# Optimization experiments

Measured on AMD Instinct MI355X. Metric: run time of the kernel, lower is better.

## Reference

```python
import jax, jax.numpy as jnp
import numpy as np

N = 50000      # num_nodes
DEG = 32       # fixed out-degree
E = N * DEG    # num graph edges
B = 1024       # num query edges (batch_size)
EPS = 1e-8
F_DROP = 0.7   # f_dropout used in random_fill


def _mlp(x, w1, b1, w2, b2):
    # Linear(1,d) -> ReLU -> Linear(d,1); x: [M,1]
    h = jax.nn.relu(x * w1[None, :] + b1[None, :])   # [M,d]
    return (h @ w2)[:, None] + b2                    # [M,1]


def setup_inputs() -> dict:
    key = jax.random.key(0)
    ks = jax.random.split(key, 20)
    inp = {
        'neighbors': jax.random.randint(ks[0], (N, DEG), 0, N, dtype=jnp.int32),
        'edge_w': jax.random.uniform(ks[1], (E,), dtype=jnp.float32),
        'src': jax.random.randint(ks[2], (B,), 0, N, dtype=jnp.int32),
        'dst': jax.random.randint(ks[3], (B,), 0, N, dtype=jnp.int32),
    }
    d = 64
    names = ['fe', 'fn', 'gp']
    i = 4
    for nm in names:
        s = 1.0 / np.sqrt(d)
        inp[nm + '_w1'] = jax.random.uniform(ks[i], (d,), minval=-1.0, maxval=1.0); i += 1
        inp[nm + '_b1'] = jax.random.uniform(ks[i], (d,), minval=-1.0, maxval=1.0); i += 1
        inp[nm + '_w2'] = jax.random.uniform(ks[i], (d,), minval=-s, maxval=s); i += 1
        inp[nm + '_b2'] = jax.random.uniform(ks[i], (1,), minval=-s, maxval=s); i += 1
    return inp


def reference(neighbors, edge_w, src, dst,
              fe_w1, fe_b1, fe_w2, fe_b2,
              fn_w1, fn_b1, fn_w2, fn_b2,
              gp_w1, gp_b1, gp_w2, gp_b2):
    # ---- node structural features: scatter_add of f_edge over edge dst ----
    cols = neighbors.reshape(-1)                                  # [E] edge dst (srcdst order)
    ew_A = _mlp(edge_w[:, None], fe_w1, fe_b1, fe_w2, fe_b2)      # [E,1]
    nsf = jnp.zeros((N, 1), dtype=ew_A.dtype).at[cols].add(ew_A)  # scatter_add -> [N,1]
    nsf = _mlp(nsf, fn_w1, fn_b1, fn_w2, fn_b2)                   # [N,1]
    nsf_v = nsf[:, 0]

    # ---- gather CSR rows for query src/dst; A.data == 1 (edge_w=False) ----
    row = jnp.repeat(jnp.arange(B, dtype=jnp.int32), DEG)         # [B*DEG]
    col_src = neighbors[src].reshape(-1)                          # [B*DEG]
    col_dst = neighbors[dst].reshape(-1)
    mat_src = jnp.zeros((B, N), dtype=nsf_v.dtype).at[row, col_src].add(nsf_v[col_src])
    mat_dst = jnp.zeros((B, N), dtype=nsf_v.dtype).at[row, col_dst].add(nsf_v[col_dst])

    # diag(mat_src @ mat_dst.T) == row-wise dot product (common neighbors)
    out_struct = jnp.sum(mat_src * mat_dst, axis=1)               # [B]

    # random_fill: add F.dropout(full(eps), p=f_dropout) -> eps/(1-p) w.p. (1-p)
    keep = 1.0 - F_DROP
    add_val = EPS / keep
    kd = jax.random.split(jax.random.key(42), 2)
    ms = mat_src + jax.random.bernoulli(kd[0], keep, (B, N)).astype(mat_src.dtype) * add_val
    md = mat_dst + jax.random.bernoulli(kd[1], keep, (B, N)).astype(mat_dst.dtype) * add_val
    D = jnp.linalg.norm(ms, axis=-1) * jnp.linalg.norm(md, axis=-1)  # [B]

    out_struct_n = _mlp((out_struct / D)[:, None], gp_w1, gp_b1, gp_w2, gp_b2)  # [B,1]
    return out_struct_n, nsf
```

## Files before the change

### kernel.cpp

```cpp
#include <hip/hip_runtime.h>

constexpr int NN   = 50000;
constexpr int KDEG = 32;
constexpr int NE   = NN * KDEG;
constexpr int NB   = 1024;
constexpr int NH   = 64;

constexpr int BINS = (NN + 255) >> 8;
constexpr int CAP  = 10240;
constexpr int EPB  = 2048;
constexpr int SCT_BLOCKS = (NE + EPB - 1) / EPB;

__device__ __forceinline__ float mlp64(float x,
                                       const float* __restrict__ w1,
                                       const float* __restrict__ b1,
                                       const float* __restrict__ w2,
                                       float b2) {
    float acc = 0.0f;
#pragma unroll 8
    for (int j = 0; j < NH; ++j) {
        float h = fmaxf(fmaf(x, w1[j], b1[j]), 0.0f);
        acc = fmaf(h, w2[j], acc);
    }
    return acc + b2;
}

__global__ __launch_bounds__(256) void scatter_kernel(
        const int* __restrict__ nbr, const float* __restrict__ ew,
        const float* __restrict__ w1, const float* __restrict__ b1,
        const float* __restrict__ w2, const float* __restrict__ b2p,
        float* __restrict__ sortedV, unsigned char* __restrict__ sortedB,
        int* __restrict__ alloc) {
    __shared__ float          sV[EPB];
    __shared__ unsigned short sN[EPB];
    __shared__ int hist[BINS];
    __shared__ int lbase[BINS + 1];
    __shared__ int gbase[BINS];

    const int tid = threadIdx.x;
    for (int i = tid; i < BINS; i += 256) hist[i] = 0;
    __syncthreads();

    const int e0 = blockIdx.x * EPB;
    const float b2 = b2p[0];
    float val[8]; int node[8]; int loc[8];
#pragma unroll
    for (int j = 0; j < 8; ++j) {
        int e = e0 + tid + j * 256;
        if (e < NE) {
            node[j] = nbr[e];
            val[j]  = mlp64(ew[e], w1, b1, w2, b2);
            loc[j]  = atomicAdd(&hist[node[j] >> 8], 1);
        } else {
            node[j] = -1;
        }
    }
    __syncthreads();

    if (tid < 64) {
        int b0 = tid * 4;
        int c0 = (b0 + 0 < BINS) ? hist[b0 + 0] : 0;
        int c1 = (b0 + 1 < BINS) ? hist[b0 + 1] : 0;
        int c2 = (b0 + 2 < BINS) ? hist[b0 + 2] : 0;
        int c3 = (b0 + 3 < BINS) ? hist[b0 + 3] : 0;
        int s = c0 + c1 + c2 + c3;
        int p = s;
#pragma unroll
        for (int off = 1; off < 64; off <<= 1) {
            int t = __shfl_up(p, off, 64);
            if (tid >= off) p += t;
        }
        int excl = p - s;
        if (b0 + 0 < BINS) lbase[b0 + 0] = excl;
        if (b0 + 1 < BINS) lbase[b0 + 1] = excl + c0;
        if (b0 + 2 < BINS) lbase[b0 + 2] = excl + c0 + c1;
        if (b0 + 3 < BINS) lbase[b0 + 3] = excl + c0 + c1 + c2;
        if (tid == 63) lbase[BINS] = p;
    }
    __syncthreads();

    if (tid < BINS) {
        int c = hist[tid];
        gbase[tid] = c ? atomicAdd(&alloc[tid], c) : 0;
    }

#pragma unroll
    for (int j = 0; j < 8; ++j) {
        if (node[j] >= 0) {
            int b = node[j] >> 8;
            int p = lbase[b] + loc[j];
            sV[p] = val[j];
            sN[p] = (unsigned short)node[j];
        }
    }
    __syncthreads();

    const int total = lbase[BINS];
    for (int j = tid; j < total; j += 256) {
        int n   = sN[j];
        int b   = n >> 8;
        int dst = gbase[b] + (j - lbase[b]);
        if (dst < CAP) {
            sortedV[(size_t)b * CAP + dst] = sV[j];
            sortedB[(size_t)b * CAP + dst] = (unsigned char)(n & 255);
        }
    }
}

__global__ __launch_bounds__(512) void reduce_kernel(
        const float* __restrict__ sortedV, const unsigned char* __restrict__ sortedB,
        const int* __restrict__ alloc,
        const float* __restrict__ w1, const float* __restrict__ b1,
        const float* __restrict__ w2, const float* __restrict__ b2p,
        float* __restrict__ nsf) {
    __shared__ float acc[256];
    const int b = blockIdx.x, tid = threadIdx.x;
    if (tid < 256) acc[tid] = 0.0f;
    __syncthreads();
    const int cnt = min(alloc[b], CAP);
    const float* pv = sortedV + (size_t)b * CAP;
    const unsigned char* pb = sortedB + (size_t)b * CAP;
    for (int i = tid; i < cnt; i += 512) {
        atomicAdd(&acc[pb[i]], pv[i]);
    }
    __syncthreads();
    if (tid < 256) {
        const int n = (b << 8) + tid;
        if (n < NN) nsf[n] = mlp64(acc[tid], w1, b1, w2, b2p[0]);
    }
}

__global__ void edge_kernel(const int* __restrict__ nbr, const float* __restrict__ ew,
                            const float* __restrict__ w1, const float* __restrict__ b1,
                            const float* __restrict__ w2, const float* __restrict__ b2p,
                            float* __restrict__ nsf0) {
    int e = blockIdx.x * blockDim.x + threadIdx.x;
    if (e >= NE) return;
    float val = mlp64(ew[e], w1, b1, w2, b2p[0]);
    atomicAdd(&nsf0[nbr[e]], val);
}

__global__ void node_kernel(float* __restrict__ nsf,
                            const float* __restrict__ w1, const float* __restrict__ b1,
                            const float* __restrict__ w2, const float* __restrict__ b2p) {
    int n = blockIdx.x * blockDim.x + threadIdx.x;
    if (n >= NN) return;
    nsf[n] = mlp64(nsf[n], w1, b1, w2, b2p[0]);
}

__global__ void pair_kernel(const int* __restrict__ nbr,
                            const int* __restrict__ src, const int* __restrict__ dst,
                            const float* __restrict__ nsf,
                            const float* __restrict__ w1, const float* __restrict__ b1,
                            const float* __restrict__ w2, const float* __restrict__ b2p,
                            float* __restrict__ out) {
    int wave = (blockIdx.x * blockDim.x + threadIdx.x) >> 6;
    int lane = threadIdx.x & 63;
    if (wave >= NB) return;

    bool isSrc = lane < 32;
    int node = isSrc ? src[wave] : dst[wave];
    int id = nbr[node * KDEG + (lane & 31)];
    float v = nsf[id];

    int cntS = 0, cntD = 0;
#pragma unroll
    for (int k = 0; k < 32; ++k) {
        int o = __shfl(id, k, 64);
        cntS += (o == id) ? 1 : 0;
    }
#pragma unroll
    for (int k = 32; k < 64; ++k) {
        int o = __shfl(id, k, 64);
        cntD += (o == id) ? 1 : 0;
    }

    float v2 = v * v;
    float dotc = isSrc ? (float)cntD * v2 : 0.0f;
    float ns   = isSrc ? (float)cntS * v2 : 0.0f;
    float nd   = isSrc ? 0.0f : (float)cntD * v2;

#pragma unroll
    for (int off = 32; off > 0; off >>= 1) {
        dotc += __shfl_xor(dotc, off, 64);
        ns   += __shfl_xor(ns,   off, 64);
        nd   += __shfl_xor(nd,   off, 64);
    }

    if (lane == 0) {
        float D = sqrtf(ns) * sqrtf(nd);
        float x = dotc / fmaxf(D, 1e-30f);
        out[wave] = mlp64(x, w1, b1, w2, b2p[0]);
    }
}

extern "C" void kernel_launch(void* const* d_in, const int* in_sizes, int n_in,
                              void* d_out, int out_size, void* d_ws, size_t ws_size,
                              hipStream_t stream) {
    const int*   nbr    = (const int*)  d_in[0];
    const float* edge_w = (const float*)d_in[1];
    const int*   src    = (const int*)  d_in[2];
    const int*   dst    = (const int*)  d_in[3];
    const float* fe_w1  = (const float*)d_in[4];
    const float* fe_b1  = (const float*)d_in[5];
    const float* fe_w2  = (const float*)d_in[6];
    const float* fe_b2  = (const float*)d_in[7];
    const float* fn_w1  = (const float*)d_in[8];
    const float* fn_b1  = (const float*)d_in[9];
    const float* fn_w2  = (const float*)d_in[10];
    const float* fn_b2  = (const float*)d_in[11];
    const float* gp_w1  = (const float*)d_in[12];
    const float* gp_b1  = (const float*)d_in[13];
    const float* gp_w2  = (const float*)d_in[14];
    const float* gp_b2  = (const float*)d_in[15];

    float* out = (float*)d_out;
    float* nsf = (float*)d_out + NB;

    const size_t nEnt    = (size_t)BINS * CAP;
    const size_t v_bytes = nEnt * sizeof(float);
    const size_t b_bytes = (nEnt + 255) & ~(size_t)255;
    const size_t need    = v_bytes + b_bytes + BINS * sizeof(int);

    if (ws_size >= need) {
        float*         sortedV = (float*)d_ws;
        unsigned char* sortedB = (unsigned char*)d_ws + v_bytes;
        int*           alloc   = (int*)((char*)d_ws + v_bytes + b_bytes);
        hipMemsetAsync(alloc, 0, BINS * sizeof(int), stream);
        scatter_kernel<<<SCT_BLOCKS, 256, 0, stream>>>(nbr, edge_w,
                                                       fe_w1, fe_b1, fe_w2, fe_b2,
                                                       sortedV, sortedB, alloc);
        reduce_kernel<<<BINS, 512, 0, stream>>>(sortedV, sortedB, alloc,
                                                fn_w1, fn_b1, fn_w2, fn_b2, nsf);
    } else {
        hipMemsetAsync(nsf, 0, (size_t)NN * sizeof(float), stream);
        edge_kernel<<<NE / 256, 256, 0, stream>>>(nbr, edge_w, fe_w1, fe_b1, fe_w2, fe_b2, nsf);
        node_kernel<<<(NN + 255) / 256, 256, 0, stream>>>(nsf, fn_w1, fn_b1, fn_w2, fn_b2);
    }

    pair_kernel<<<(NB * 64) / 256, 256, 0, stream>>>(nbr, src, dst, nsf,
                                                     gp_w1, gp_b1, gp_w2, gp_b2, out);
}
```

Before: 137.8 us.

## Replace global atomic bin allocation with fixed per-block bin cells

Each scatter block now writes its sorted edges for every node bin into a fixed cell of up to 40 slots, indexed by bin and block, plus a per-cell byte count. This replaces the global atomic offset allocation and removes the memset. The reduce kernel, now 1024 threads per block, has each thread walk one cell serially. The edge MLP helper also gets two independent accumulators for more instruction-level parallelism. The trade-offs: a much larger workspace, strided and partly filled cell reads in the reduce, and silent truncation if a block ever sends more than 40 edges to one bin.

Result: faster. 126.7 us (-8.0%).

```diff
diff --git a/kernel.cpp b/kernel.cpp
--- a/kernel.cpp
+++ b/kernel.cpp
@@ -7,22 +7,24 @@
 constexpr int NH   = 64;
 
 constexpr int BINS = (NN + 255) >> 8;
-constexpr int CAP  = 10240;
 constexpr int EPB  = 2048;
 constexpr int SCT_BLOCKS = (NE + EPB - 1) / EPB;
+constexpr int CAP2 = 40;
 
 __device__ __forceinline__ float mlp64(float x,
                                        const float* __restrict__ w1,
                                        const float* __restrict__ b1,
                                        const float* __restrict__ w2,
                                        float b2) {
-    float acc = 0.0f;
+    float a0 = 0.0f, a1 = 0.0f;
 #pragma unroll 8
-    for (int j = 0; j < NH; ++j) {
-        float h = fmaxf(fmaf(x, w1[j], b1[j]), 0.0f);
-        acc = fmaf(h, w2[j], acc);
-    }
-    return acc + b2;
+    for (int j = 0; j < NH; j += 2) {
+        float h0 = fmaxf(fmaf(x, w1[j],     b1[j]),     0.0f);
+        float h1 = fmaxf(fmaf(x, w1[j + 1], b1[j + 1]), 0.0f);
+        a0 = fmaf(h0, w2[j],     a0);
+        a1 = fmaf(h1, w2[j + 1], a1);
+    }
+    return a0 + a1 + b2;
 }
 
 __global__ __launch_bounds__(256) void scatter_kernel(
@@ -30,18 +32,18 @@
         const float* __restrict__ w1, const float* __restrict__ b1,
         const float* __restrict__ w2, const float* __restrict__ b2p,
         float* __restrict__ sortedV, unsigned char* __restrict__ sortedB,
-        int* __restrict__ alloc) {
+        unsigned char* __restrict__ cnt) {
     __shared__ float          sV[EPB];
     __shared__ unsigned short sN[EPB];
     __shared__ int hist[BINS];
     __shared__ int lbase[BINS + 1];
-    __shared__ int gbase[BINS];
 
     const int tid = threadIdx.x;
+    const int blk = blockIdx.x;
     for (int i = tid; i < BINS; i += 256) hist[i] = 0;
     __syncthreads();
 
-    const int e0 = blockIdx.x * EPB;
+    const int e0 = blk * EPB;
     const float b2 = b2p[0];
     float val[8]; int node[8]; int loc[8];
 #pragma unroll
@@ -77,12 +79,11 @@
         if (b0 + 3 < BINS) lbase[b0 + 3] = excl + c0 + c1 + c2;
         if (tid == 63) lbase[BINS] = p;
     }
-    __syncthreads();
-
     if (tid < BINS) {
-        int c = hist[tid];
-        gbase[tid] = c ? atomicAdd(&alloc[tid], c) : 0;
-    }
+        cnt[(size_t)tid * SCT_BLOCKS + blk] =
+            (unsigned char)min(hist[tid], CAP2);
+    }
+    __syncthreads();
 
 #pragma unroll
     for (int j = 0; j < 8; ++j) {
@@ -97,35 +98,37 @@
 
     const int total = lbase[BINS];
     for (int j = tid; j < total; j += 256) {
-        int n   = sN[j];
-        int b   = n >> 8;
-        int dst = gbase[b] + (j - lbase[b]);
-        if (dst < CAP) {
-            sortedV[(size_t)b * CAP + dst] = sV[j];
-            sortedB[(size_t)b * CAP + dst] = (unsigned char)(n & 255);
-        }
-    }
-}
-
-__global__ __launch_bounds__(512) void reduce_kernel(
+        int n    = sN[j];
+        int b    = n >> 8;
+        int slot = j - lbase[b];
+        if (slot < CAP2) {
+            size_t base = ((size_t)b * SCT_BLOCKS + blk) * CAP2 + slot;
+            sortedV[base] = sV[j];
+            sortedB[base] = (unsigned char)(n & 255);
+        }
+    }
+}
+
+__global__ __launch_bounds__(1024) void reduce_kernel(
         const float* __restrict__ sortedV, const unsigned char* __restrict__ sortedB,
-        const int* __restrict__ alloc,
+        const unsigned char* __restrict__ cnt,
         const float* __restrict__ w1, const float* __restrict__ b1,
         const float* __restrict__ w2, const float* __restrict__ b2p,
         float* __restrict__ nsf) {
     __shared__ float acc[256];
-    const int b = blockIdx.x, tid = threadIdx.x;
+    const int bin = blockIdx.x, tid = threadIdx.x;
     if (tid < 256) acc[tid] = 0.0f;
     __syncthreads();
-    const int cnt = min(alloc[b], CAP);
-    const float* pv = sortedV + (size_t)b * CAP;
-    const unsigned char* pb = sortedB + (size_t)b * CAP;
-    for (int i = tid; i < cnt; i += 512) {
-        atomicAdd(&acc[pb[i]], pv[i]);
+    for (int cell = tid; cell < SCT_BLOCKS; cell += 1024) {
+        int c = cnt[(size_t)bin * SCT_BLOCKS + cell];
+        size_t base = ((size_t)bin * SCT_BLOCKS + cell) * CAP2;
+        for (int k = 0; k < c; ++k) {
+            atomicAdd(&acc[sortedB[base + k]], sortedV[base + k]);
+        }
     }
     __syncthreads();
     if (tid < 256) {
-        const int n = (b << 8) + tid;
+        const int n = (bin << 8) + tid;
         if (n < NN) nsf[n] = mlp64(acc[tid], w1, b1, w2, b2p[0]);
     }
 }
@@ -217,21 +220,21 @@
     float* out = (float*)d_out;
     float* nsf = (float*)d_out + NB;
 
-    const size_t nEnt    = (size_t)BINS * CAP;
-    const size_t v_bytes = nEnt * sizeof(float);
-    const size_t b_bytes = (nEnt + 255) & ~(size_t)255;
-    const size_t need    = v_bytes + b_bytes + BINS * sizeof(int);
+    const size_t nCells  = (size_t)BINS * SCT_BLOCKS;
+    const size_t v_bytes = nCells * CAP2 * sizeof(float);
+    const size_t b_bytes = (nCells * CAP2 + 255) & ~(size_t)255;
+    const size_t c_bytes = (nCells + 255) & ~(size_t)255;
+    const size_t need    = v_bytes + b_bytes + c_bytes;
 
     if (ws_size >= need) {
         float*         sortedV = (float*)d_ws;
         unsigned char* sortedB = (unsigned char*)d_ws + v_bytes;
-        int*           alloc   = (int*)((char*)d_ws + v_bytes + b_bytes);
-        hipMemsetAsync(alloc, 0, BINS * sizeof(int), stream);
+        unsigned char* cnt     = (unsigned char*)d_ws + v_bytes + b_bytes;
         scatter_kernel<<<SCT_BLOCKS, 256, 0, stream>>>(nbr, edge_w,
                                                        fe_w1, fe_b1, fe_w2, fe_b2,
-                                                       sortedV, sortedB, alloc);
-        reduce_kernel<<<BINS, 512, 0, stream>>>(sortedV, sortedB, alloc,
-                                                fn_w1, fn_b1, fn_w2, fn_b2, nsf);
+                                                       sortedV, sortedB, cnt);
+        reduce_kernel<<<BINS, 1024, 0, stream>>>(sortedV, sortedB, cnt,
+                                                 fn_w1, fn_b1, fn_w2, fn_b2, nsf);
     } else {
         hipMemsetAsync(nsf, 0, (size_t)NN * sizeof(float), stream);
         edge_kernel<<<NE / 256, 256, 0, stream>>>(nbr, edge_w, fe_w1, fe_b1, fe_w2, fe_b2, nsf);
```
